# Kernel optimization log

Measured on AMD Instinct MI355X. Metric: run time of the kernel, lower is better.

Reference implementation:

```python
import jax, jax.numpy as jnp
import numpy as np

DOMAIN_MIN, DOMAIN_MAX = -1.0, 1.0
N, D_IN, D_OUT, K = 1024, 128, 128, 8


def setup_inputs() -> dict:
    key = jax.random.key(0)
    k1, k2, k3 = jax.random.split(key, 3)
    x = jax.random.uniform(k1, (N, D_IN), dtype=jnp.float32,
                           minval=DOMAIN_MIN, maxval=DOMAIN_MAX)
    # Per-edge spline knot values: near-identity init plus small noise.
    base = jnp.linspace(DOMAIN_MIN, DOMAIN_MAX, K, dtype=jnp.float32)
    coeffs = base[None, None, :] + 0.1 * jax.random.normal(
        k2, (D_OUT, D_IN, K), dtype=jnp.float32)
    weights = jax.random.normal(k3, (D_OUT, D_IN), dtype=jnp.float32) * np.sqrt(2.0 / D_IN)
    bias = jnp.zeros((D_OUT,), dtype=jnp.float32)
    return {"x": x, "coeffs": coeffs, "weights": weights, "bias": bias}


def _spline_all_edges(x, coeffs):
    """Evaluate every edge's cubic (Catmull-Rom) spline at its input.
    x: [N, d_in]; coeffs: [d_out, d_in, K] knot values on uniform knots in [-1,1].
    Returns s: [N, d_in, d_out]."""
    K_ = coeffs.shape[-1]
    h = (DOMAIN_MAX - DOMAIN_MIN) / (K_ - 1)
    xc = jnp.clip(x, DOMAIN_MIN, DOMAIN_MAX)
    t = (xc - DOMAIN_MIN) / h                      # [N, d_in], in [0, K-1]
    idx = jnp.clip(jnp.floor(t).astype(jnp.int32), 0, K_ - 2)
    u = t - idx                                    # local coord in [0,1]
    i0 = jnp.clip(idx - 1, 0, K_ - 1)
    i1 = idx
    i2 = idx + 1
    i3 = jnp.clip(idx + 2, 0, K_ - 1)
    ct = jnp.transpose(coeffs, (1, 2, 0))          # [d_in, K, d_out]
    jar = jnp.arange(ct.shape[0])[None, :]          # [1, d_in]
    p0 = ct[jar, i0]                               # [N, d_in, d_out]
    p1 = ct[jar, i1]
    p2 = ct[jar, i2]
    p3 = ct[jar, i3]
    u2 = u * u
    u3 = u2 * u
    b0 = 0.5 * (-u3 + 2.0 * u2 - u)
    b1 = 0.5 * (3.0 * u3 - 5.0 * u2 + 2.0)
    b2 = 0.5 * (-3.0 * u3 + 4.0 * u2 + u)
    b3 = 0.5 * (u3 - u2)
    return (b0[..., None] * p0 + b1[..., None] * p1 +
            b2[..., None] * p2 + b3[..., None] * p3)


def reference(x, coeffs, weights, bias):
    # h_i(x) = sum_j w_ij * s_ij(x_j) + b_i
    s = _spline_all_edges(x, coeffs)               # [N, d_in, d_out]
    return jnp.einsum('njo,oj->no', s, weights) + bias[None, :]
```

## Files before the change

kernel.cpp:

```cpp
#include <hip/hip_runtime.h>
#include <hip/hip_bf16.h>
#include <stdint.h>


#define DIN 128
#define DOUT 128
#define KTOT 1024

typedef unsigned int u32;
typedef unsigned short u16;
typedef __attribute__((ext_vector_type(8))) short bf16x8;
typedef __attribute__((ext_vector_type(4))) float f32x4;

union H8 { u16 s[8]; uint4 v; };

__device__ __forceinline__ u16 f2b(float f) {
    union { __hip_bfloat16 h; u16 u; } c;
    c.h = __float2bfloat16(f);
    return c.u;
}

__global__ __launch_bounds__(1024) void kan_fused(
    const float* __restrict__ x, const float* __restrict__ coeffs,
    const float* __restrict__ weights, const float* __restrict__ bias,
    float* __restrict__ out)
{
    __shared__ __align__(16) u16 sBas[16 * KTOT];
    __shared__ __align__(16) u16 sWp [16 * KTOT];
    float* sC = (float*)sBas;

    const int tid  = threadIdx.x;
    const int wave = tid >> 6;
    const int lane = tid & 63;
    const int n0 = blockIdx.x * 16;
    const int o0 = blockIdx.y * 16;

    #pragma unroll
    for (int it = 0; it < 2; ++it) {
        const int task = tid + it * 1024;
        const int row = task >> 7;
        const int j = task & 127;
        float xv = x[n0 * DIN + task];
        xv = fminf(fmaxf(xv, -1.0f), 1.0f);
        const float t = (xv + 1.0f) * 3.5f;
        int idx = (int)t; idx = idx > 6 ? 6 : idx;
        const float u = t - (float)idx;
        const float u2 = u * u, u3 = u2 * u;
        const float b0 = 0.5f * (-u3 + 2.0f * u2 - u);
        const float b1 = 0.5f * (3.0f * u3 - 5.0f * u2 + 2.0f);
        const float b2 = 0.5f * (-3.0f * u3 + 4.0f * u2 + u);
        const float b3 = 0.5f * (u3 - u2);
        float r[8];
        #pragma unroll
        for (int k = 0; k < 8; ++k) r[k] = 0.0f;
        const int i0 = idx > 0 ? idx - 1 : 0;
        const int i3 = idx < 6 ? idx + 2 : 7;
        r[i0] += b0; r[idx] += b1; r[idx + 1] += b2; r[i3] += b3;
        H8 h;
        #pragma unroll
        for (int k = 0; k < 8; ++k) h.s[k] = f2b(r[k]);
        const int uu = j ^ (row & 7);
        *(uint4*)(sBas + row * KTOT + uu * 8) = h.v;
    }

    #pragma unroll
    for (int it = 0; it < 2; ++it) {
        const int task = tid + it * 1024;
        const int o = task >> 7;
        const int j = task & 127;
        const float wv = weights[o0 * DIN + task];
        const float4 c0 = *(const float4*)(coeffs + o0 * KTOT + task * 8);
        const float4 c1 = *(const float4*)(coeffs + o0 * KTOT + task * 8 + 4);
        H8 h;
        h.s[0] = f2b(c0.x * wv); h.s[1] = f2b(c0.y * wv);
        h.s[2] = f2b(c0.z * wv); h.s[3] = f2b(c0.w * wv);
        h.s[4] = f2b(c1.x * wv); h.s[5] = f2b(c1.y * wv);
        h.s[6] = f2b(c1.z * wv); h.s[7] = f2b(c1.w * wv);
        const int uu = j ^ (o & 7);
        *(uint4*)(sWp + o * KTOT + uu * 8) = h.v;
    }
    __syncthreads();

    const int mo = lane & 15;
    const int q  = lane >> 4;
    const int sw = mo & 7;
    f32x4 acc = {0.0f, 0.0f, 0.0f, 0.0f};
    #pragma unroll
    for (int s = 0; s < 2; ++s) {
        const int S = wave * 2 + s;
        const int uu = (S * 4 + q) ^ sw;
        bf16x8 af = *(const bf16x8*)(sBas + mo * KTOT + uu * 8);
        bf16x8 bf = *(const bf16x8*)(sWp  + mo * KTOT + uu * 8);
        acc = __builtin_amdgcn_mfma_f32_16x16x32_bf16(af, bf, acc, 0, 0, 0);
    }
    __syncthreads();

    #pragma unroll
    for (int r = 0; r < 4; ++r)
        sC[wave * 256 + (q * 4 + r) * 16 + mo] = acc[r];
    __syncthreads();

    if (tid < 256) {
        const int row = tid >> 4, col = tid & 15;
        float v = sC[tid];
        #pragma unroll
        for (int w = 1; w < 16; ++w) v += sC[w * 256 + tid];
        out[(n0 + row) * DOUT + o0 + col] = v + bias[o0 + col];
    }
}

extern "C" void kernel_launch(void* const* d_in, const int* in_sizes, int n_in,
                              void* d_out, int out_size, void* d_ws, size_t ws_size,
                              hipStream_t stream) {
    const float* x       = (const float*)d_in[0];
    const float* coeffs  = (const float*)d_in[1];
    const float* weights = (const float*)d_in[2];
    const float* bias    = (const float*)d_in[3];
    float* out = (float*)d_out;
    const int N = in_sizes[0] / DIN;
    dim3 grid(N / 16, DOUT / 16);
    kan_fused<<<grid, 1024, 0, stream>>>(x, coeffs, weights, bias, out);
}
```

Before: 62.50 us.

## Precompute bf16 weighted coefficients in prep kernel and remap blocks per XCD

A separate prep kernel multiplies the coefficients by the edge weights once and stores them as bf16 in the workspace. The main kernel then copies that compact tile into shared memory instead of reloading fp32 coefficients and redoing the scaling in each of the 64 row blocks. The grid becomes 1D with a swizzled mapping that groups row/output tiles per XCD, aiming for better L2 reuse. This adds a second kernel launch and a workspace round trip, and hardcodes N=1024 (512 blocks).

After: 63.98 us. 2.4% more time.

```diff
diff --git a/kernel.cpp b/kernel.cpp
--- a/kernel.cpp
+++ b/kernel.cpp
@@ -20,10 +20,25 @@
     return c.u;
 }
 
+__global__ __launch_bounds__(256) void kan_wprep(
+    const float* __restrict__ coeffs, const float* __restrict__ weights,
+    u16* __restrict__ wsW)
+{
+    const int gid = blockIdx.x * 256 + threadIdx.x;
+    const float wv = weights[gid];
+    const float4 c0 = *(const float4*)(coeffs + gid * 8);
+    const float4 c1 = *(const float4*)(coeffs + gid * 8 + 4);
+    H8 h;
+    h.s[0] = f2b(c0.x * wv); h.s[1] = f2b(c0.y * wv);
+    h.s[2] = f2b(c0.z * wv); h.s[3] = f2b(c0.w * wv);
+    h.s[4] = f2b(c1.x * wv); h.s[5] = f2b(c1.y * wv);
+    h.s[6] = f2b(c1.z * wv); h.s[7] = f2b(c1.w * wv);
+    *(uint4*)(wsW + gid * 8) = h.v;
+}
+
 __global__ __launch_bounds__(1024) void kan_fused(
-    const float* __restrict__ x, const float* __restrict__ coeffs,
-    const float* __restrict__ weights, const float* __restrict__ bias,
-    float* __restrict__ out)
+    const float* __restrict__ x, const u16* __restrict__ wsW,
+    const float* __restrict__ bias, float* __restrict__ out)
 {
     __shared__ __align__(16) u16 sBas[16 * KTOT];
     __shared__ __align__(16) u16 sWp [16 * KTOT];
@@ -32,8 +47,14 @@
     const int tid  = threadIdx.x;
     const int wave = tid >> 6;
     const int lane = tid & 63;
-    const int n0 = blockIdx.x * 16;
-    const int o0 = blockIdx.y * 16;
+
+    const int id  = blockIdx.x;
+    const int xcd = id & 7;
+    const int loc = id >> 3;
+    const int mt = ((xcd >> 1) << 4) | (loc & 15);
+    const int ot = ((xcd & 1) << 2) | (loc >> 4);
+    const int n0 = mt * 16;
+    const int o0 = ot * 16;
 
     #pragma unroll
     for (int it = 0; it < 2; ++it) {
@@ -66,18 +87,11 @@
     #pragma unroll
     for (int it = 0; it < 2; ++it) {
         const int task = tid + it * 1024;
-        const int o = task >> 7;
-        const int j = task & 127;
-        const float wv = weights[o0 * DIN + task];
-        const float4 c0 = *(const float4*)(coeffs + o0 * KTOT + task * 8);
-        const float4 c1 = *(const float4*)(coeffs + o0 * KTOT + task * 8 + 4);
-        H8 h;
-        h.s[0] = f2b(c0.x * wv); h.s[1] = f2b(c0.y * wv);
-        h.s[2] = f2b(c0.z * wv); h.s[3] = f2b(c0.w * wv);
-        h.s[4] = f2b(c1.x * wv); h.s[5] = f2b(c1.y * wv);
-        h.s[6] = f2b(c1.z * wv); h.s[7] = f2b(c1.w * wv);
-        const int uu = j ^ (o & 7);
-        *(uint4*)(sWp + o * KTOT + uu * 8) = h.v;
+        const int row = task >> 7;
+        const int u0 = task & 127;
+        const uint4 v = *(const uint4*)(wsW + (o0 + row) * KTOT + u0 * 8);
+        const int uu = u0 ^ (row & 7);
+        *(uint4*)(sWp + row * KTOT + uu * 8) = v;
     }
     __syncthreads();
 
@@ -117,7 +131,7 @@
     const float* weights = (const float*)d_in[2];
     const float* bias    = (const float*)d_in[3];
     float* out = (float*)d_out;
-    const int N = in_sizes[0] / DIN;
-    dim3 grid(N / 16, DOUT / 16);
-    kan_fused<<<grid, 1024, 0, stream>>>(x, coeffs, weights, bias, out);
+    u16* wsW = (u16*)d_ws;
+    kan_wprep<<<DOUT * DIN / 256, 256, 0, stream>>>(coeffs, weights, wsW);
+    kan_fused<<<512, 1024, 0, stream>>>(x, wsW, bias, out);
 }
```
